# Kernel tuning notes

Measured on AMD Instinct MI355X. Metric: run time of the kernel, lower is better.

Reference implementation:

```python
import jax, jax.numpy as jnp
import numpy as np

COMMITMENT_COST = 0.25


def setup_inputs() -> dict:
    key = jax.random.key(0)
    k1, k2 = jax.random.split(key)
    inputs = jax.random.normal(k1, (32, 1024, 256), dtype=jnp.float32)
    codebook = jax.random.normal(k2, (8192, 256), dtype=jnp.float32)
    return {"inputs": inputs, "codebook": codebook}


def reference(inputs, codebook):
    input_shape = inputs.shape
    D = codebook.shape[1]
    K = codebook.shape[0]
    flat = inputs.reshape(-1, D)                      # [N, D]
    N = flat.shape[0]

    distances = (
        jnp.sum(flat * flat, axis=1, keepdims=True)
        + jnp.sum(codebook * codebook, axis=1)
        - 2.0 * flat @ codebook.T
    )                                                  # [N, K]
    idx = jnp.argmin(distances, axis=1)               # [N]

    # gather (equivalent to one-hot @ codebook)
    quantized = jnp.take(codebook, idx, axis=0).reshape(input_shape)

    # straight-through estimator
    quantized_st = inputs + jax.lax.stop_gradient(quantized - inputs)

    e_latent_loss = jnp.mean((jax.lax.stop_gradient(quantized_st) - inputs) ** 2)
    q_latent_loss = jnp.mean((quantized - jax.lax.stop_gradient(inputs)) ** 2)
    commitment_loss = COMMITMENT_COST * e_latent_loss
    codebook_loss = q_latent_loss
    vq_loss = commitment_loss + codebook_loss

    # perplexity of codebook usage (avg one-hot probs)
    counts = jnp.zeros((K,), dtype=inputs.dtype).at[idx].add(1.0)
    avg_probs = counts / N
    perplexity = jnp.exp(-jnp.sum(avg_probs * jnp.log(avg_probs + 1e-10)))

    tokens = idx.reshape(input_shape[:-1])
    return quantized_st, tokens, vq_loss, commitment_loss, codebook_loss, perplexity
```

## Files before the change

### kernel.cpp

```cpp
#include <hip/hip_runtime.h>
#include <stdint.h>

typedef unsigned short u16;
typedef unsigned long long u64;

#define N_ROWS 32768
#define DIM 256
#define K_CODES 8192
#define TAU 0.3f

#define A_OFF     0ull
#define B_OFF     16777216ull
#define CN_OFF    20971520ull
#define PART1_OFF 21004288ull
#define PART2_OFF 22052864ull
#define IDX_OFF   22577152ull
#define HIST_OFF  22708224ull
#define CNT_OFF   22740992ull
#define FLAG_OFF  22741008ull
#define LOSS_OFF  22872080ull
#define CBT_OFF   23068672ull
#define GMIN2_OFF 31457280ull

#define OUT_Q 0
#define OUT_T 8388608
#define OUT_S 8421376

#define BM 128
#define BN 128
#define BK 64
#define JSPLIT 2
#define NT (4 * ((K_CODES / JSPLIT) / BN))
#define RSPLIT 4
#define RGRID 512

#define PACK_INF ((((u64)0xFF800000u) << 32) | 0xFFFFFFFFull)

typedef _Float16 half8 __attribute__((ext_vector_type(8)));
typedef float floatx4 __attribute__((ext_vector_type(4)));

__device__ __forceinline__ void gload_lds16(const void* g, void* l) {
    __builtin_amdgcn_global_load_lds(
        (const __attribute__((address_space(1))) void*)g,
        (__attribute__((address_space(3))) void*)l,
        16, 0, 0);
}

__device__ __forceinline__ unsigned sortable(float v) {
    unsigned u = __float_as_uint(v);
    return (u & 0x80000000u) ? ~u : (u | 0x80000000u);
}
__device__ __forceinline__ float unsortable(unsigned u) {
    return (u & 0x80000000u) ? __uint_as_float(u & 0x7fffffffu) : __uint_as_float(~u);
}
__device__ __forceinline__ u64 shfl64x(u64 v, int m) {
    return ((u64)(unsigned)__shfl_xor((int)(v >> 32), m, 64) << 32) |
           (unsigned)__shfl_xor((int)(v & 0xffffffffu), m, 64);
}
__device__ __forceinline__ u64 u64min(u64 a, u64 b) { return a < b ? a : b; }
__device__ __forceinline__ u64 u64max(u64 a, u64 b) { return a > b ? a : b; }

__global__ void prep(const float* __restrict__ inp, const float* __restrict__ cb,
                     u16* __restrict__ A, u16* __restrict__ B, float* __restrict__ cn,
                     unsigned int* __restrict__ hist, int* __restrict__ cnt,
                     float* __restrict__ cbT) {
    __shared__ float tile[64][65];
    const int tid = threadIdx.x;

    if (blockIdx.x >= 5153) {
        const int bx = blockIdx.x - 5153;
        const int tj = (bx & 127) * 64;
        const int td = (bx >> 7) * 64;
        const int c = (tid & 15) * 4;
        const int r0 = tid >> 4;
#pragma unroll
        for (int p = 0; p < 4; ++p) {
            int r = p * 16 + r0;
            float4 v = *(const float4*)(cb + (size_t)(tj + r) * DIM + td + c);
            tile[r][c] = v.x; tile[r][c + 1] = v.y; tile[r][c + 2] = v.z; tile[r][c + 3] = v.w;
        }
        __syncthreads();
#pragma unroll
        for (int p = 0; p < 4; ++p) {
            int rr = p * 16 + r0;
            float4 w = {tile[c][rr], tile[c + 1][rr], tile[c + 2][rr], tile[c + 3][rr]};
            *(float4*)(cbT + (size_t)(td + rr) * K_CODES + tj + c) = w;
        }
        return;
    }
    if (blockIdx.x >= 5120) {
        int i = (blockIdx.x - 5120) * 256 + tid;
        if (i < K_CODES) hist[i] = 0u;
        else if (i < K_CODES + 4) cnt[i - K_CODES] = 0;
        return;
    }
    int g = blockIdx.x * 256 + tid;
    int row = g >> 5;
    int kc = (g & 31) << 3;
    bool isA = row < N_ROWS;
    const float* src = isA ? inp + (size_t)row * DIM + kc
                           : cb + (size_t)(row - N_ROWS) * DIM + kc;
    u16* dst = isA ? A + (size_t)row * DIM + kc
                   : B + (size_t)(row - N_ROWS) * DIM + kc;
    float4 x0 = *(const float4*)(src);
    float4 x1 = *(const float4*)(src + 4);
    float xs[8] = {x0.x, x0.y, x0.z, x0.w, x1.x, x1.y, x1.z, x1.w};
    half8 hv;
    float s = 0.f;
#pragma unroll
    for (int i = 0; i < 8; ++i) {
        hv[i] = (_Float16)xs[i];
        s = fmaf(xs[i], xs[i], s);
    }
    *(half8*)(dst) = hv;
    if (!isA) {
#pragma unroll
        for (int m = 1; m <= 16; m <<= 1) s += __shfl_xor(s, m, 64);
        if ((g & 31) == 0) cn[row - N_ROWS] = s;
    }
}

#define STAGE_T(T, BUFI)                                                      \
    {                                                                         \
        const int jc_ = (T) >> 2;                                             \
        const int kk_ = ((T) & 3) * BK;                                       \
        const int colBase_ = jBase + jc_ * BN;                                \
        _Pragma("unroll")                                                     \
        for (int it_ = 0; it_ < 4; ++it_) {                                   \
            int r_ = it_ * 32 + str;                                          \
            int cdat_ = sk16 ^ (r_ & 7);                                      \
            int ch_ = it_ * 256 + tid;                                        \
            gload_lds16(A + (size_t)(rowBase + r_) * DIM + kk_ + cdat_ * 8,   \
                        (char*)lsA[BUFI] + ch_ * 16);                         \
            gload_lds16(B + (size_t)(colBase_ + r_) * DIM + kk_ + cdat_ * 8,  \
                        (char*)lsB[BUFI] + ch_ * 16);                         \
        }                                                                     \
    }

#define TOP2NI(JC, NI)                                                        \
    {                                                                         \
        unsigned j_ = (unsigned)(jBase + (JC) * BN + wn * 64 + (NI) * 16 + l15); \
        float cnj_ = cn[j_];                                                  \
        _Pragma("unroll")                                                     \
        for (int mi_ = 0; mi_ < 4; ++mi_) {                                   \
            _Pragma("unroll")                                                 \
            for (int r_ = 0; r_ < 4; ++r_) {                                  \
                int tr_ = mi_ * 4 + r_;                                       \
                float val_ = fmaf(-2.0f, acc[mi_][NI][r_], cnj_);             \
                float nd2_ = __builtin_amdgcn_fmed3f(d1[tr_], d2[tr_], val_); \
                bool lt_ = val_ < d1[tr_];                                    \
                d1[tr_] = fminf(d1[tr_], val_);                               \
                idxr[tr_] = lt_ ? j_ : idxr[tr_];                             \
                d2[tr_] = nd2_;                                               \
            }                                                                 \
        }                                                                     \
    }

__launch_bounds__(256, 2)
__global__ void vq_pass1(const u16* __restrict__ A, const u16* __restrict__ B,
                         const float* __restrict__ cn,
                         u64* __restrict__ part1, float* __restrict__ part2) {
    __shared__ __align__(16) _Float16 lsA[2][BM * BK];
    __shared__ __align__(16) _Float16 lsB[2][BN * BK];
    __shared__ u64 t1buf[BM];
    __shared__ float t2buf[BM];

    const int tid = threadIdx.x;
    const int lane = tid & 63;
    const int w = tid >> 6;
    const int wm = w >> 1, wn = w & 1;
    const int l15 = lane & 15;
    const int quad = lane >> 4;
    const int xm = l15 & 7;
    const int rowBase = blockIdx.x * BM;
    const int jBase = blockIdx.y * (K_CODES / JSPLIT);

    float d1[16], d2[16];
    unsigned idxr[16];
#pragma unroll
    for (int i = 0; i < 16; ++i) {
        d1[i] = __builtin_inff(); d2[i] = __builtin_inff(); idxr[i] = 0xffffffffu;
    }

    const int str = tid >> 3;
    const int sk16 = tid & 7;

    STAGE_T(0, 0);
    asm volatile("s_waitcnt vmcnt(0)" ::: "memory");
    __builtin_amdgcn_s_barrier();
    asm volatile("" ::: "memory");

    floatx4 acc[4][4];
    int buf = 0;

#pragma unroll 1
    for (int t = 0; t < NT; ++t) {
        if (t + 1 < NT) STAGE_T(t + 1, buf ^ 1);

        if ((t & 3) == 0) {
            if (t >= 4) {
                TOP2NI((t >> 2) - 1, 2);
                TOP2NI((t >> 2) - 1, 3);
            }
#pragma unroll
            for (int mi = 0; mi < 4; ++mi)
#pragma unroll
                for (int ni = 0; ni < 4; ++ni)
                    acc[mi][ni] = (floatx4){0.f, 0.f, 0.f, 0.f};
        }

#pragma unroll
        for (int s = 0; s < 2; ++s) {
            const int koff = ((s * 4 + quad) ^ xm) * 8;
            half8 af[4], bf[4];
#pragma unroll
            for (int mi = 0; mi < 4; ++mi)
                af[mi] = *(const half8*)(lsA[buf] + (wm * 64 + mi * 16 + l15) * BK + koff);
#pragma unroll
            for (int ni = 0; ni < 4; ++ni)
                bf[ni] = *(const half8*)(lsB[buf] + (wn * 64 + ni * 16 + l15) * BK + koff);
#pragma unroll
            for (int mi = 0; mi < 4; ++mi)
#pragma unroll
                for (int ni = 0; ni < 4; ++ni)
                    acc[mi][ni] = __builtin_amdgcn_mfma_f32_16x16x32_f16(
                        af[mi], bf[ni], acc[mi][ni], 0, 0, 0);
        }

        if ((t & 3) == 3) {
            TOP2NI(t >> 2, 0);
            TOP2NI(t >> 2, 1);
        }

        asm volatile("s_waitcnt vmcnt(0)" ::: "memory");
        __builtin_amdgcn_s_barrier();
        asm volatile("" ::: "memory");
        buf ^= 1;
    }
    TOP2NI((NT >> 2) - 1, 2);
    TOP2NI((NT >> 2) - 1, 3);

    u64 m1[16];
#pragma unroll
    for (int tr = 0; tr < 16; ++tr)
        m1[tr] = ((u64)sortable(d1[tr]) << 32) | idxr[tr];
#pragma unroll
    for (int m = 1; m <= 8; m <<= 1)
#pragma unroll
        for (int tr = 0; tr < 16; ++tr) {
            u64 o1 = shfl64x(m1[tr], m);
            float o2 = __shfl_xor(d2[tr], m, 64);
            u64 n1 = u64min(m1[tr], o1);
            float big = unsortable((unsigned)(u64max(m1[tr], o1) >> 32));
            d2[tr] = fminf(big, fminf(d2[tr], o2));
            m1[tr] = n1;
        }

    if (wn == 0 && l15 == 0) {
#pragma unroll
        for (int tr = 0; tr < 16; ++tr) {
            int rl = wm * 64 + (tr >> 2) * 16 + quad * 4 + (tr & 3);
            t1buf[rl] = m1[tr]; t2buf[rl] = d2[tr];
        }
    }
    __syncthreads();
    if (wn == 1 && l15 == 0) {
#pragma unroll
        for (int tr = 0; tr < 16; ++tr) {
            int rl = wm * 64 + (tr >> 2) * 16 + quad * 4 + (tr & 3);
            u64 o1 = t1buf[rl];
            float o2 = t2buf[rl];
            u64 n1 = u64min(m1[tr], o1);
            float big = unsortable((unsigned)(u64max(m1[tr], o1) >> 32));
            float n2 = fminf(big, fminf(d2[tr], o2));
            size_t p = (size_t)(rowBase + rl) * JSPLIT + blockIdx.y;
            part1[p] = n1;
            part2[p] = n2;
        }
    }
}

__global__ void vq_merge(const u64* __restrict__ part1, const float* __restrict__ part2,
                         unsigned* __restrict__ idx32,
                         int* __restrict__ flaglist, int* __restrict__ cnt,
                         u64* __restrict__ gmin2) {
    int row = blockIdx.x * 256 + threadIdx.x;
    u64 m1 = PACK_INF;
    float f2 = __builtin_inff();
#pragma unroll
    for (int y = 0; y < JSPLIT; ++y) {
        u64 p1 = part1[(size_t)row * JSPLIT + y];
        float p2 = part2[(size_t)row * JSPLIT + y];
        u64 n1 = u64min(m1, p1);
        float big = unsortable((unsigned)(u64max(m1, p1) >> 32));
        f2 = fminf(big, fminf(f2, p2));
        m1 = n1;
    }
    gmin2[row] = PACK_INF;
    idx32[row] = (unsigned)(m1 & 0xffffffffu);
    float f1 = unsortable((unsigned)(m1 >> 32));
    if (f2 - f1 < TAU) {
        int p = atomicAdd(cnt, 1);
        flaglist[p] = row;
    }
}

__global__ void vq_recompute(const float* __restrict__ inp, const float* __restrict__ cbT,
                             const float* __restrict__ cn, const int* __restrict__ flaglist,
                             const int* __restrict__ cnt, u64* __restrict__ gmin2) {
    __shared__ float xsT[DIM][8];
    __shared__ u64 wred[8][8];
    const int tid = threadIdx.x;
    const int w = tid >> 6, lane = tid & 63;
    const int n = *cnt;
    const int cbase = blockIdx.y * (K_CODES / RSPLIT) + tid * 4;

#pragma unroll 1
    for (int base = blockIdx.x * 8; base < n; base += RGRID * 8) {
        {
            int li = base + w;
            int row = flaglist[li < n ? li : (n - 1)];
            float4 a = ((const float4*)(inp + (size_t)row * DIM))[lane];
            int d0 = lane * 4;
            xsT[d0 + 0][w] = a.x; xsT[d0 + 1][w] = a.y;
            xsT[d0 + 2][w] = a.z; xsT[d0 + 3][w] = a.w;
        }
        __syncthreads();

        float4 acc[8];
#pragma unroll
        for (int r = 0; r < 8; ++r) acc[r] = (float4){0.f, 0.f, 0.f, 0.f};

        float4 cv = *(const float4*)(cbT + cbase);
#pragma unroll 4
        for (int d = 0; d < DIM - 1; ++d) {
            float4 nx = *(const float4*)(cbT + (size_t)(d + 1) * K_CODES + cbase);
            float4 xa = *(const float4*)&xsT[d][0];
            float4 xb = *(const float4*)&xsT[d][4];
            float xv[8] = {xa.x, xa.y, xa.z, xa.w, xb.x, xb.y, xb.z, xb.w};
#pragma unroll
            for (int r = 0; r < 8; ++r) {
                acc[r].x = fmaf(xv[r], cv.x, acc[r].x);
                acc[r].y = fmaf(xv[r], cv.y, acc[r].y);
                acc[r].z = fmaf(xv[r], cv.z, acc[r].z);
                acc[r].w = fmaf(xv[r], cv.w, acc[r].w);
            }
            cv = nx;
        }
        {
            const int d = DIM - 1;
            float4 xa = *(const float4*)&xsT[d][0];
            float4 xb = *(const float4*)&xsT[d][4];
            float xv[8] = {xa.x, xa.y, xa.z, xa.w, xb.x, xb.y, xb.z, xb.w};
#pragma unroll
            for (int r = 0; r < 8; ++r) {
                acc[r].x = fmaf(xv[r], cv.x, acc[r].x);
                acc[r].y = fmaf(xv[r], cv.y, acc[r].y);
                acc[r].z = fmaf(xv[r], cv.z, acc[r].z);
                acc[r].w = fmaf(xv[r], cv.w, acc[r].w);
            }
        }

        u64 best[8];
        float4 cn4 = *(const float4*)(cn + cbase);
#pragma unroll
        for (int r = 0; r < 8; ++r) {
            float e0 = cn4.x - 2.0f * acc[r].x;
            float e1 = cn4.y - 2.0f * acc[r].y;
            float e2 = cn4.z - 2.0f * acc[r].z;
            float e3 = cn4.w - 2.0f * acc[r].w;
            u64 b = ((u64)sortable(e0) << 32) | (unsigned)(cbase + 0);
            b = u64min(b, ((u64)sortable(e1) << 32) | (unsigned)(cbase + 1));
            b = u64min(b, ((u64)sortable(e2) << 32) | (unsigned)(cbase + 2));
            b = u64min(b, ((u64)sortable(e3) << 32) | (unsigned)(cbase + 3));
            best[r] = b;
        }

#pragma unroll
        for (int m = 1; m <= 32; m <<= 1)
#pragma unroll
            for (int r = 0; r < 8; ++r) best[r] = u64min(best[r], shfl64x(best[r], m));
        if (lane < 8) wred[w][lane] = best[lane];
        __syncthreads();
        if (tid < 8 && base + tid < n) {
            u64 b = wred[0][tid];
#pragma unroll
            for (int ww = 1; ww < 8; ++ww) b = u64min(b, wred[ww][tid]);
            atomicMin(&gmin2[flaglist[base + tid]], b);
        }
    }
}

__global__ void vq_gather(const float* __restrict__ inp, const float* __restrict__ cb,
                          const unsigned* __restrict__ idx32,
                          const u64* __restrict__ gmin2, float* __restrict__ out,
                          float* __restrict__ losspart, unsigned int* __restrict__ hist) {
    __shared__ float red[4];
    int w = threadIdx.x >> 6, lane = threadIdx.x & 63;
    int i = blockIdx.x * 4 + w;
    unsigned idx = idx32[i];
    u64 g = gmin2[i];
    if (g != PACK_INF) idx = (unsigned)(g & 0xffffffffull);
    float4 c = ((const float4*)(cb + (size_t)idx * DIM))[lane];
    float4 x = ((const float4*)(inp + (size_t)i * DIM))[lane];
    ((float4*)(out + OUT_Q))[(size_t)i * 64 + lane] = c;
    float dx = c.x - x.x, dy = c.y - x.y, dz = c.z - x.z, dw = c.w - x.w;
    float s = dx * dx + dy * dy + dz * dz + dw * dw;
#pragma unroll
    for (int m = 32; m; m >>= 1) s += __shfl_xor(s, m, 64);
    if (lane == 0) {
        out[OUT_T + i] = (float)idx;
        red[w] = s;
        atomicAdd(&hist[idx], 1u);
    }
    __syncthreads();
    if (threadIdx.x == 0)
        losspart[blockIdx.x] = red[0] + red[1] + red[2] + red[3];
}

__global__ void vq_finalize(const unsigned int* __restrict__ hist,
                            const float* __restrict__ losspart, float* __restrict__ out) {
    __shared__ float redp[256], redl[256];
    int tid = threadIdx.x;
    float sp = 0.f, sl = 0.f;
    for (int k = tid; k < K_CODES; k += 256) {
        float p = (float)hist[k] * (1.0f / (float)N_ROWS);
        sp += p * logf(p + 1e-10f);
        sl += losspart[k];
    }
    redp[tid] = sp; redl[tid] = sl;
    __syncthreads();
    for (int st = 128; st; st >>= 1) {
        if (tid < st) { redp[tid] += redp[tid + st]; redl[tid] += redl[tid + st]; }
        __syncthreads();
    }
    if (tid == 0) {
        float perp = expf(-redp[0]);
        float e = redl[0] / 8388608.0f;
        out[OUT_S + 0] = 1.25f * e;
        out[OUT_S + 1] = 0.25f * e;
        out[OUT_S + 2] = e;
        out[OUT_S + 3] = perp;
    }
}

extern "C" void kernel_launch(void* const* d_in, const int* in_sizes, int n_in,
                              void* d_out, int out_size, void* d_ws, size_t ws_size,
                              hipStream_t stream) {
    const float* inp = (const float*)d_in[0];
    const float* cb = (const float*)d_in[1];
    float* out = (float*)d_out;
    char* ws = (char*)d_ws;
    u16* A = (u16*)(ws + A_OFF);
    u16* B = (u16*)(ws + B_OFF);
    float* cn = (float*)(ws + CN_OFF);
    u64* part1 = (u64*)(ws + PART1_OFF);
    float* part2 = (float*)(ws + PART2_OFF);
    unsigned* idx32 = (unsigned*)(ws + IDX_OFF);
    unsigned int* hist = (unsigned int*)(ws + HIST_OFF);
    int* cnt = (int*)(ws + CNT_OFF);
    int* flaglist = (int*)(ws + FLAG_OFF);
    float* losspart = (float*)(ws + LOSS_OFF);
    float* cbT = (float*)(ws + CBT_OFF);
    u64* gmin2 = (u64*)(ws + GMIN2_OFF);

    prep<<<5665, 256, 0, stream>>>(inp, cb, A, B, cn, hist, cnt, cbT);
    vq_pass1<<<dim3(N_ROWS / BM, JSPLIT), 256, 0, stream>>>(A, B, cn, part1, part2);
    vq_merge<<<N_ROWS / 256, 256, 0, stream>>>(part1, part2, idx32, flaglist, cnt, gmin2);
    vq_recompute<<<dim3(RGRID, RSPLIT), 512, 0, stream>>>(inp, cbT, cn, flaglist, cnt, gmin2);
    vq_gather<<<N_ROWS / 4, 256, 0, stream>>>(inp, cb, idx32, gmin2, out, losspart, hist);
    vq_finalize<<<1, 256, 0, stream>>>(hist, losspart, out);
}
```

Baseline: 390.7 us.

## Split codebook across four column groups and evaluate top-2 in one epilogue

Raises the codebook split from two to four column groups, so the grid has twice as many blocks and each block scans half as many codes. The top-2 distance update, previously split across two points of the loop to overlap with the next tile's MFMAs, now runs all four column fragments at the end of each column tile. It also adds a barrier in the refinement loop and clamps the gathered index as a safety measure. The change trades the old overlap of epilogue work for more parallelism, but produces twice as many partial results to merge afterward.

```diff
diff --git a/kernel.cpp b/kernel.cpp
--- a/kernel.cpp
+++ b/kernel.cpp
@@ -29,7 +29,7 @@
 #define BM 128
 #define BN 128
 #define BK 64
-#define JSPLIT 2
+#define JSPLIT 4
 #define NT (4 * ((K_CODES / JSPLIT) / BN))
 #define RSPLIT 4
 #define RGRID 512
@@ -137,25 +137,6 @@
         }                                                                     \
     }
 
-#define TOP2NI(JC, NI)                                                        \
-    {                                                                         \
-        unsigned j_ = (unsigned)(jBase + (JC) * BN + wn * 64 + (NI) * 16 + l15); \
-        float cnj_ = cn[j_];                                                  \
-        _Pragma("unroll")                                                     \
-        for (int mi_ = 0; mi_ < 4; ++mi_) {                                   \
-            _Pragma("unroll")                                                 \
-            for (int r_ = 0; r_ < 4; ++r_) {                                  \
-                int tr_ = mi_ * 4 + r_;                                       \
-                float val_ = fmaf(-2.0f, acc[mi_][NI][r_], cnj_);             \
-                float nd2_ = __builtin_amdgcn_fmed3f(d1[tr_], d2[tr_], val_); \
-                bool lt_ = val_ < d1[tr_];                                    \
-                d1[tr_] = fminf(d1[tr_], val_);                               \
-                idxr[tr_] = lt_ ? j_ : idxr[tr_];                             \
-                d2[tr_] = nd2_;                                               \
-            }                                                                 \
-        }                                                                     \
-    }
-
 __launch_bounds__(256, 2)
 __global__ void vq_pass1(const u16* __restrict__ A, const u16* __restrict__ B,
                          const float* __restrict__ cn,
@@ -198,10 +179,6 @@
         if (t + 1 < NT) STAGE_T(t + 1, buf ^ 1);
 
         if ((t & 3) == 0) {
-            if (t >= 4) {
-                TOP2NI((t >> 2) - 1, 2);
-                TOP2NI((t >> 2) - 1, 3);
-            }
 #pragma unroll
             for (int mi = 0; mi < 4; ++mi)
 #pragma unroll
@@ -228,8 +205,25 @@
         }
 
         if ((t & 3) == 3) {
-            TOP2NI(t >> 2, 0);
-            TOP2NI(t >> 2, 1);
+            const int colBase = jBase + (t >> 2) * BN;
+#pragma unroll
+            for (int ni = 0; ni < 4; ++ni) {
+                unsigned j = (unsigned)(colBase + wn * 64 + ni * 16 + l15);
+                float cnj = cn[j];
+#pragma unroll
+                for (int mi = 0; mi < 4; ++mi) {
+#pragma unroll
+                    for (int r = 0; r < 4; ++r) {
+                        int tr = mi * 4 + r;
+                        float val = fmaf(-2.0f, acc[mi][ni][r], cnj);
+                        float nd2 = __builtin_amdgcn_fmed3f(d1[tr], d2[tr], val);
+                        bool lt = val < d1[tr];
+                        d1[tr] = fminf(d1[tr], val);
+                        idxr[tr] = lt ? j : idxr[tr];
+                        d2[tr] = nd2;
+                    }
+                }
+            }
         }
 
         asm volatile("s_waitcnt vmcnt(0)" ::: "memory");
@@ -237,8 +231,6 @@
         asm volatile("" ::: "memory");
         buf ^= 1;
     }
-    TOP2NI((NT >> 2) - 1, 2);
-    TOP2NI((NT >> 2) - 1, 3);
 
     u64 m1[16];
 #pragma unroll
@@ -388,6 +380,7 @@
             for (int ww = 1; ww < 8; ++ww) b = u64min(b, wred[ww][tid]);
             atomicMin(&gmin2[flaglist[base + tid]], b);
         }
+        __syncthreads();
     }
 }
 
@@ -401,6 +394,7 @@
     unsigned idx = idx32[i];
     u64 g = gmin2[i];
     if (g != PACK_INF) idx = (unsigned)(g & 0xffffffffull);
+    if (idx >= K_CODES) idx = K_CODES - 1;
     float4 c = ((const float4*)(cb + (size_t)idx * DIM))[lane];
     float4 x = ((const float4*)(inp + (size_t)i * DIM))[lane];
     ((float4*)(out + OUT_Q))[(size_t)i * 64 + lane] = c;
```

Result: slower. 403.1 us (+3.2%).
